# Kernel optimization log

Measured on AMD Instinct MI355X. Metric: run time of the kernel, lower is better.

The kernel has to match this reference:

```python
import jax, jax.numpy as jnp
import numpy as np

HIDDEN = 1024
HEADS = 16
HEAD_DIM = HIDDEN // HEADS


def setup_inputs() -> dict:
    key = jax.random.key(0)
    ks = jax.random.split(key, 9)
    s = 1.0 / np.sqrt(HIDDEN)
    return {
        "x": jax.random.normal(ks[0], (2, 2048, HIDDEN), dtype=jnp.float32),
        "Wq": jax.random.uniform(ks[1], (HIDDEN, HIDDEN), jnp.float32, -s, s),
        "bq": jax.random.uniform(ks[2], (HIDDEN,), jnp.float32, -s, s),
        "Wk": jax.random.uniform(ks[3], (HIDDEN, HIDDEN), jnp.float32, -s, s),
        "bk": jax.random.uniform(ks[4], (HIDDEN,), jnp.float32, -s, s),
        "Wv": jax.random.uniform(ks[5], (HIDDEN, HIDDEN), jnp.float32, -s, s),
        "bv": jax.random.uniform(ks[6], (HIDDEN,), jnp.float32, -s, s),
        "Wo": jax.random.uniform(ks[7], (HIDDEN, HIDDEN), jnp.float32, -s, s),
        "bo": jax.random.uniform(ks[8], (HIDDEN,), jnp.float32, -s, s),
    }


def reference(x, Wq, bq, Wk, bk, Wv, bv, Wo, bo):
    B, N, C = x.shape
    H, D = HEADS, HEAD_DIM
    # torch Linear: y = x @ W.T + b; weights here stored as (out, in)
    q = (x @ Wq.T + bq).reshape(B, N, H, D).transpose(0, 2, 1, 3)  # bhnd
    k = (x @ Wk.T + bk).reshape(B, N, H, D).transpose(0, 2, 1, 3)
    v = (x @ Wv.T + bv).reshape(B, N, H, D).transpose(0, 2, 1, 3)
    scale = D ** -0.5
    attn = jnp.einsum("bhnd,bhmd->bhnm", q, k) * scale
    attn = jax.nn.softmax(attn, axis=-1)
    out = jnp.einsum("bhnm,bhmd->bhnd", attn, v)
    out = out.transpose(0, 2, 1, 3).reshape(B, N, C)
    return out @ Wo.T + bo
```

## Files before the change

kernel.cpp:

```cpp
#include <hip/hip_runtime.h>
#include <stdint.h>

#define HIDDEN 1024
#define HEADS 16
#define HEAD_DIM 64
#define NBATCH 2
#define SEQ 2048

typedef short bh8 __attribute__((ext_vector_type(8)));
typedef _Float16 hf4 __attribute__((ext_vector_type(4)));
typedef _Float16 hf8 __attribute__((ext_vector_type(8)));
typedef float fx4 __attribute__((ext_vector_type(4)));

#define MFMA_BF16(a, b, c) __builtin_amdgcn_mfma_f32_16x16x32_bf16((a), (b), (c), 0, 0, 0)
#define MFMA_F16_16(a, b, c) __builtin_amdgcn_mfma_f32_16x16x16f16((a), (b), (c), 0, 0, 0)

__device__ __forceinline__ short f2bf(float f) {
  union { float f; uint32_t u; } v; v.f = f;
  uint32_t r = v.u + 0x7fffu + ((v.u >> 16) & 1u);
  return (short)(r >> 16);
}
__device__ __forceinline__ short f2h(float f) {
  union { _Float16 h; short s; } v; v.h = (_Float16)f;
  return v.s;
}

typedef __attribute__((address_space(1))) void GV;
typedef __attribute__((address_space(3))) void LV;
__device__ __forceinline__ void gl_lds16(const void* g, void* l) {
  __builtin_amdgcn_global_load_lds((GV*)g, (LV*)l, 16, 0, 0);
}

__device__ __forceinline__ size_t img_off(int row, int k) {
  int rt = row >> 7, kt = k >> 6;
  int g = (((row & 127) >> 4) << 1) + ((k & 63) >> 5);
  int l = (((k & 31) >> 3) << 4) + (row & 15);
  return ((size_t)((rt * 16 + kt) * 16 + g) << 9) + (l << 3) + (k & 7);
}

__global__ void cvt_kernel(const float* __restrict__ x,
                           const float* __restrict__ wq, const float* __restrict__ wk,
                           const float* __restrict__ wv, const float* __restrict__ wo,
                           short* __restrict__ xb, short* __restrict__ wqb,
                           short* __restrict__ wkb, short* __restrict__ wvb,
                           short* __restrict__ wob) {
  long t = (long)blockIdx.x * blockDim.x + threadIdx.x;
  long i = t * 8;
  const float* s; short* d; long off;
  if (i < 4194304L) { s = x; d = xb; off = i; }
  else {
    long j = i - 4194304L;
    int w = (int)(j >> 20);
    off = j & 1048575L;
    s = (w == 0) ? wq : (w == 1) ? wk : (w == 2) ? wv : wo;
    d = (w == 0) ? wqb : (w == 1) ? wkb : (w == 2) ? wvb : wob;
  }
  float4 v0 = *(const float4*)(s + off);
  float4 v1 = *(const float4*)(s + off + 4);
  bh8 o;
  o[0] = f2bf(v0.x); o[1] = f2bf(v0.y); o[2] = f2bf(v0.z); o[3] = f2bf(v0.w);
  o[4] = f2bf(v1.x); o[5] = f2bf(v1.y); o[6] = f2bf(v1.z); o[7] = f2bf(v1.w);
  int row = (int)(off >> 10), k = (int)(off & 1023);
  *(bh8*)(d + img_off(row, k)) = o;
}

__global__ __launch_bounds__(256)
void qkv_kernel(const short* __restrict__ xb,
                const short* __restrict__ wqb, const short* __restrict__ wkb,
                const short* __restrict__ wvb,
                const float* __restrict__ bq, const float* __restrict__ bk,
                const float* __restrict__ bv,
                short* __restrict__ Q, short* __restrict__ K, short* __restrict__ Vt) {
  __shared__ __align__(16) short smem[16384];
  short* Alds = smem;
  short* Blds = smem + 8192;

  const int lin = blockIdx.x;
  const int xcd = lin & 7, idx = lin >> 3;
  const int mt = (xcd >> 1) * 8 + (idx & 7);
  const int zo = (xcd & 1) * 12 + (idx >> 3);
  const int z = zo >> 3, ot = zo & 7;

  const short* W = (z == 0) ? wqb : (z == 1) ? wkb : wvb;
  const float* bias = (z == 0) ? bq : (z == 1) ? bk : bv;
  const int tid = threadIdx.x;
  const int lane = tid & 63, w = tid >> 6;
  const int r = lane & 15, q = lane >> 4;
  const int wr = w >> 1, wc = w & 1;

  fx4 acc[4][4] = {};

  for (int kt = 0; kt < 16; ++kt) {
#pragma unroll
    for (int i = 0; i < 4; ++i) {
      int c = w * 4 + i;
      gl_lds16(xb + (((size_t)(mt * 16 + kt) * 16 + c) << 9) + lane * 8,
               (char*)Alds + c * 1024);
      gl_lds16(W + (((size_t)(ot * 16 + kt) * 16 + c) << 9) + lane * 8,
               (char*)Blds + c * 1024);
    }
    __syncthreads();
#pragma unroll
    for (int ks = 0; ks < 2; ++ks) {
      bh8 af[4], bf_[4];
#pragma unroll
      for (int ti = 0; ti < 4; ++ti)
        af[ti] = *(const bh8*)&Alds[(((wr * 4 + ti) * 2 + ks) << 9) + lane * 8];
#pragma unroll
      for (int tj = 0; tj < 4; ++tj)
        bf_[tj] = *(const bh8*)&Blds[(((wc * 4 + tj) * 2 + ks) << 9) + lane * 8];
#pragma unroll
      for (int ti = 0; ti < 4; ++ti)
#pragma unroll
        for (int tj = 0; tj < 4; ++tj)
          acc[ti][tj] = MFMA_BF16(af[ti], bf_[tj], acc[ti][tj]);
    }
    __syncthreads();
  }

  const float QS = 0.18033688011112042f;
#pragma unroll
  for (int ti = 0; ti < 4; ++ti)
#pragma unroll
    for (int tj = 0; tj < 4; ++tj)
#pragma unroll
      for (int i = 0; i < 4; ++i) {
        int nl = wr * 64 + ti * 16 + q * 4 + i;
        int cl = wc * 64 + tj * 16 + r;
        int hl = cl >> 6, d = cl & 63;
        float v = acc[ti][tj][i] + bias[ot * 128 + cl];
        short sv; int lo;
        if (z == 0) {
          sv = f2bf(v * QS);
          lo = hl * 8192 + nl * 64 + d;
        } else if (z == 1) {
          sv = f2bf(v);
          int g = ((nl >> 4) << 1) + (d >> 5);
          int lp = (((d & 31) >> 3) << 4) + (nl & 15);
          lo = hl * 8192 + g * 512 + lp * 8 + (d & 7);
        } else {
          sv = f2h(v);
          int dt = d >> 4, rp = d & 15;
          int ks2 = nl >> 4, pi = ks2 >> 1, hh = ks2 & 1;
          int qp = (nl & 15) >> 2, ii = nl & 3;
          lo = hl * 8192 + (dt * 4 + pi) * 512 + (qp * 16 + rp) * 8 + hh * 4 + ii;
        }
        smem[lo] = sv;
      }
  __syncthreads();
  {
    int b = mt >> 4;
    int n0 = (mt & 15) * 128;
    int jj = mt & 15;
    short* dst = (z == 0) ? Q : (z == 1) ? K : Vt;
#pragma unroll
    for (int kk = 0; kk < 8; ++kk) {
      int s = kk * 256 + tid;
      int hl = s >> 10, inner = s & 1023;
      int bh = b * 16 + ot * 2 + hl;
      size_t go = (size_t)bh * 131072 +
                  (z == 0 ? (size_t)n0 * 64 : (size_t)jj * 8192) + (size_t)inner * 8;
      *(int4*)(dst + go) = *(const int4*)(smem + (size_t)s * 8);
    }
  }
}

__global__ __launch_bounds__(512, 4)
void attn_kernel(const short* __restrict__ Q, const short* __restrict__ Kf,
                 const short* __restrict__ Vf, short* __restrict__ A) {
  __shared__ __align__(16) short Klds[2][8192];
  __shared__ __align__(16) short Vlds[2][8192];

  const int lin = blockIdx.x;
  const int xcd = lin & 7, idx = lin >> 3;
  const int bh = xcd + 8 * (idx & 3);
  const int n0 = (idx >> 2) * 128;

  const int tid = threadIdx.x;
  const int lane = tid & 63, w = tid >> 6;
  const int r = lane & 15, q = lane >> 4;

  const short* Qg = Q + (size_t)bh * 131072;
  const short* Kg = Kf + (size_t)bh * 131072;
  const short* Vg = Vf + (size_t)bh * 131072;

  bh8 qf[2];
#pragma unroll
  for (int ks = 0; ks < 2; ++ks)
    qf[ks] = *(const bh8*)(Qg + (size_t)(n0 + w * 16 + r) * 64 + ks * 32 + q * 8);

  fx4 o[4] = {};
  float l_run = 0.f;

#define ATTN_STAGE(j, b)                                                        \
  {                                                                             \
    const short* ktp = Kg + (j) * 8192;                                         \
    const short* vtp = Vg + (j) * 8192;                                         \
    _Pragma("unroll") for (int i = 0; i < 4; ++i) {                             \
      if (w < 4) {                                                              \
        int c = w * 4 + i;                                                      \
        gl_lds16(ktp + c * 512 + lane * 8, (char*)&Klds[b][0] + c * 1024);      \
      } else {                                                                  \
        int c = (w - 4) * 4 + i;                                                \
        gl_lds16(vtp + c * 512 + lane * 8, (char*)&Vlds[b][0] + c * 1024);      \
      }                                                                         \
    }                                                                           \
  }

  ATTN_STAGE(0, 0);
  __syncthreads();

  for (int j = 0; j < 16; ++j) {
    int cur = j & 1;
    if (j < 15) ATTN_STAGE(j + 1, cur ^ 1);

    fx4 s[8] = {};
#pragma unroll
    for (int ks = 0; ks < 2; ++ks)
#pragma unroll
      for (int tj = 0; tj < 8; ++tj) {
        bh8 kf = *(const bh8*)&Klds[cur][(tj * 2 + ks) * 512 + lane * 8];
        s[tj] = MFMA_BF16(kf, qf[ks], s[tj]);
      }

    hf4 p[8];
#pragma unroll
    for (int tj = 0; tj < 8; ++tj)
#pragma unroll
      for (int i = 0; i < 4; ++i) {
        float e = __builtin_amdgcn_exp2f(s[tj][i]);
        l_run += e;
        p[tj][i] = (_Float16)e;
      }

#pragma unroll
    for (int pi = 0; pi < 4; ++pi)
#pragma unroll
      for (int dt = 0; dt < 4; ++dt) {
        hf8 vv = *(const hf8*)&Vlds[cur][(dt * 4 + pi) * 512 + lane * 8];
        hf4 vlo = __builtin_shufflevector(vv, vv, 0, 1, 2, 3);
        hf4 vhi = __builtin_shufflevector(vv, vv, 4, 5, 6, 7);
        o[dt] = MFMA_F16_16(vlo, p[2 * pi], o[dt]);
        o[dt] = MFMA_F16_16(vhi, p[2 * pi + 1], o[dt]);
      }
    __syncthreads();
  }
#undef ATTN_STAGE

  float l = l_run;
  l += __shfl_xor(l, 16);
  l += __shfl_xor(l, 32);
  const float inv = 1.0f / l;

  const int h = bh & 15;
  const int mt = (bh >> 4) * 16 + (n0 >> 7);
#pragma unroll
  for (int dt = 0; dt < 4; ++dt) {
    short4 ov;
    ov.x = f2bf(o[dt][0] * inv);
    ov.y = f2bf(o[dt][1] * inv);
    ov.z = f2bf(o[dt][2] * inv);
    ov.w = f2bf(o[dt][3] * inv);
    int g = w * 2 + (dt >> 1);
    int lp = ((dt & 1) * 2 + (q >> 1)) * 16 + r;
    *(short4*)(A + (((size_t)(mt * 16 + h) * 16 + g) << 9) + lp * 8 + (q & 1) * 4) = ov;
  }
}

__global__ __launch_bounds__(256)
void proj_kernel(const short* __restrict__ ab, const short* __restrict__ wob,
                 const float* __restrict__ bo, float* __restrict__ out) {
  __shared__ __align__(16) short Alds[4096];
  __shared__ __align__(16) short Blds[4096];

  const int lin = blockIdx.x;
  const int xcd = lin & 7, idx = lin >> 3;
  const int mt = xcd * 8 + (idx & 7);
  const int ot = idx >> 3;

  const int tid = threadIdx.x;
  const int lane = tid & 63, w = tid >> 6;
  const int r = lane & 15, q = lane >> 4;
  const int wm = w & 1, wn = w >> 1;
  const int rt = mt >> 1, rh = mt & 1;
  const int st = ot >> 1, sh = ot & 1;

  fx4 acc[2][2] = {};

  for (int kt = 0; kt < 16; ++kt) {
#pragma unroll
    for (int i = 0; i < 2; ++i) {
      int c = w * 2 + i;
      gl_lds16(ab + (((size_t)(rt * 16 + kt) * 16 + rh * 8 + c) << 9) + lane * 8,
               (char*)Alds + c * 1024);
      gl_lds16(wob + (((size_t)(st * 16 + kt) * 16 + sh * 8 + c) << 9) + lane * 8,
               (char*)Blds + c * 1024);
    }
    __syncthreads();
#pragma unroll
    for (int ks = 0; ks < 2; ++ks) {
      bh8 af[2], bf_[2];
#pragma unroll
      for (int tm = 0; tm < 2; ++tm)
        af[tm] = *(const bh8*)&Alds[(((wm * 2 + tm) * 2 + ks) << 9) + lane * 8];
#pragma unroll
      for (int tn = 0; tn < 2; ++tn)
        bf_[tn] = *(const bh8*)&Blds[(((wn * 2 + tn) * 2 + ks) << 9) + lane * 8];
#pragma unroll
      for (int tm = 0; tm < 2; ++tm)
#pragma unroll
        for (int tn = 0; tn < 2; ++tn)
          acc[tm][tn] = MFMA_BF16(af[tm], bf_[tn], acc[tm][tn]);
    }
    __syncthreads();
  }

#pragma unroll
  for (int tm = 0; tm < 2; ++tm)
#pragma unroll
    for (int tn = 0; tn < 2; ++tn)
#pragma unroll
      for (int i = 0; i < 4; ++i) {
        int row = mt * 64 + wm * 32 + tm * 16 + q * 4 + i;
        int col = ot * 64 + wn * 32 + tn * 16 + r;
        out[(size_t)row * 1024 + col] = acc[tm][tn][i] + bo[col];
      }
}

extern "C" void kernel_launch(void* const* d_in, const int* in_sizes, int n_in,
                              void* d_out, int out_size, void* d_ws, size_t ws_size,
                              hipStream_t stream) {
  const float* x  = (const float*)d_in[0];
  const float* Wq = (const float*)d_in[1];
  const float* bq = (const float*)d_in[2];
  const float* Wk = (const float*)d_in[3];
  const float* bk = (const float*)d_in[4];
  const float* Wv = (const float*)d_in[5];
  const float* bv = (const float*)d_in[6];
  const float* Wo = (const float*)d_in[7];
  const float* bo = (const float*)d_in[8];
  float* out = (float*)d_out;
  char* ws = (char*)d_ws;

  short* xb  = (short*)(ws);
  short* wqb = (short*)(ws + 8388608);
  short* wkb = (short*)(ws + 8388608 + 2097152);
  short* wvb = (short*)(ws + 8388608 + 2 * 2097152);
  short* wob = (short*)(ws + 8388608 + 3 * 2097152);
  short* Qb  = (short*)(ws + 16777216);
  short* Kb  = (short*)(ws + 16777216 + 8388608);
  short* Vtb = (short*)(ws + 16777216 + 2 * 8388608);
  short* Ab  = (short*)(ws);

  cvt_kernel<<<4096, 256, 0, stream>>>(x, Wq, Wk, Wv, Wo, xb, wqb, wkb, wvb, wob);
  qkv_kernel<<<768, 256, 0, stream>>>(xb, wqb, wkb, wvb, bq, bk, bv, Qb, Kb, Vtb);
  attn_kernel<<<512, 512, 0, stream>>>(Qb, Kb, Vtb, Ab);
  proj_kernel<<<1024, 256, 0, stream>>>(Ab, wob, bo, out);
}
```

Baseline: 198.4 us.

## Double-buffer LDS tiles in QKV and projection GEMMs, widen QKV blocks to 8 waves

```diff
diff --git a/kernel.cpp b/kernel.cpp
--- a/kernel.cpp
+++ b/kernel.cpp
@@ -64,16 +64,14 @@
   *(bh8*)(d + img_off(row, k)) = o;
 }
 
-__global__ __launch_bounds__(256)
+__global__ __launch_bounds__(512)
 void qkv_kernel(const short* __restrict__ xb,
                 const short* __restrict__ wqb, const short* __restrict__ wkb,
                 const short* __restrict__ wvb,
                 const float* __restrict__ bq, const float* __restrict__ bk,
                 const float* __restrict__ bv,
                 short* __restrict__ Q, short* __restrict__ K, short* __restrict__ Vt) {
-  __shared__ __align__(16) short smem[16384];
-  short* Alds = smem;
-  short* Blds = smem + 8192;
+  __shared__ __align__(16) short smem[32768];
 
   const int lin = blockIdx.x;
   const int xcd = lin & 7, idx = lin >> 3;
@@ -86,49 +84,61 @@
   const int tid = threadIdx.x;
   const int lane = tid & 63, w = tid >> 6;
   const int r = lane & 15, q = lane >> 4;
-  const int wr = w >> 1, wc = w & 1;
-
-  fx4 acc[4][4] = {};
+  const int wr = w & 3, wc = w >> 2;
+
+  fx4 acc[2][4] = {};
+
+#define QKV_STAGE(kt, b)                                                            \
+  {                                                                                 \
+    _Pragma("unroll") for (int i = 0; i < 4; ++i) {                                 \
+      int c = w * 4 + i;                                                            \
+      if (c < 16)                                                                   \
+        gl_lds16(xb + (((size_t)(mt * 16 + (kt)) * 16 + c) << 9) + lane * 8,        \
+                 (char*)smem + (size_t)(b) * 16384 + c * 1024);                     \
+      else                                                                          \
+        gl_lds16(W + (((size_t)(ot * 16 + (kt)) * 16 + (c - 16)) << 9) + lane * 8,  \
+                 (char*)smem + 32768 + (size_t)(b) * 16384 + (c - 16) * 1024);      \
+    }                                                                               \
+  }
+
+  QKV_STAGE(0, 0);
+  __syncthreads();
 
   for (int kt = 0; kt < 16; ++kt) {
-#pragma unroll
-    for (int i = 0; i < 4; ++i) {
-      int c = w * 4 + i;
-      gl_lds16(xb + (((size_t)(mt * 16 + kt) * 16 + c) << 9) + lane * 8,
-               (char*)Alds + c * 1024);
-      gl_lds16(W + (((size_t)(ot * 16 + kt) * 16 + c) << 9) + lane * 8,
-               (char*)Blds + c * 1024);
+    int cur = kt & 1;
+    if (kt < 15) QKV_STAGE(kt + 1, cur ^ 1);
+    const short* Ab_ = smem + cur * 8192;
+    const short* Bb_ = smem + 16384 + cur * 8192;
+#pragma unroll
+    for (int ks = 0; ks < 2; ++ks) {
+      bh8 af[2], bf_[4];
+#pragma unroll
+      for (int tm = 0; tm < 2; ++tm)
+        af[tm] = *(const bh8*)&Ab_[(((wr * 2 + tm) * 2 + ks) << 9) + lane * 8];
+#pragma unroll
+      for (int tn = 0; tn < 4; ++tn)
+        bf_[tn] = *(const bh8*)&Bb_[(((wc * 4 + tn) * 2 + ks) << 9) + lane * 8];
+#pragma unroll
+      for (int tm = 0; tm < 2; ++tm)
+#pragma unroll
+        for (int tn = 0; tn < 4; ++tn)
+          acc[tm][tn] = MFMA_BF16(af[tm], bf_[tn], acc[tm][tn]);
     }
     __syncthreads();
-#pragma unroll
-    for (int ks = 0; ks < 2; ++ks) {
-      bh8 af[4], bf_[4];
-#pragma unroll
-      for (int ti = 0; ti < 4; ++ti)
-        af[ti] = *(const bh8*)&Alds[(((wr * 4 + ti) * 2 + ks) << 9) + lane * 8];
-#pragma unroll
-      for (int tj = 0; tj < 4; ++tj)
-        bf_[tj] = *(const bh8*)&Blds[(((wc * 4 + tj) * 2 + ks) << 9) + lane * 8];
-#pragma unroll
-      for (int ti = 0; ti < 4; ++ti)
-#pragma unroll
-        for (int tj = 0; tj < 4; ++tj)
-          acc[ti][tj] = MFMA_BF16(af[ti], bf_[tj], acc[ti][tj]);
-    }
-    __syncthreads();
-  }
+  }
+#undef QKV_STAGE
 
   const float QS = 0.18033688011112042f;
 #pragma unroll
-  for (int ti = 0; ti < 4; ++ti)
-#pragma unroll
-    for (int tj = 0; tj < 4; ++tj)
+  for (int tm = 0; tm < 2; ++tm)
+#pragma unroll
+    for (int tn = 0; tn < 4; ++tn)
 #pragma unroll
       for (int i = 0; i < 4; ++i) {
-        int nl = wr * 64 + ti * 16 + q * 4 + i;
-        int cl = wc * 64 + tj * 16 + r;
+        int nl = wr * 32 + tm * 16 + q * 4 + i;
+        int cl = wc * 64 + tn * 16 + r;
         int hl = cl >> 6, d = cl & 63;
-        float v = acc[ti][tj][i] + bias[ot * 128 + cl];
+        float v = acc[tm][tn][i] + bias[ot * 128 + cl];
         short sv; int lo;
         if (z == 0) {
           sv = f2bf(v * QS);
@@ -154,8 +164,8 @@
     int jj = mt & 15;
     short* dst = (z == 0) ? Q : (z == 1) ? K : Vt;
 #pragma unroll
-    for (int kk = 0; kk < 8; ++kk) {
-      int s = kk * 256 + tid;
+    for (int kk = 0; kk < 4; ++kk) {
+      int s = kk * 512 + tid;
       int hl = s >> 10, inner = s & 1023;
       int bh = b * 16 + ot * 2 + hl;
       size_t go = (size_t)bh * 131072 +
@@ -270,8 +280,8 @@
 __global__ __launch_bounds__(256)
 void proj_kernel(const short* __restrict__ ab, const short* __restrict__ wob,
                  const float* __restrict__ bo, float* __restrict__ out) {
-  __shared__ __align__(16) short Alds[4096];
-  __shared__ __align__(16) short Blds[4096];
+  __shared__ __align__(16) short Alds[2][4096];
+  __shared__ __align__(16) short Blds[2][4096];
 
   const int lin = blockIdx.x;
   const int xcd = lin & 7, idx = lin >> 3;
@@ -287,25 +297,34 @@
 
   fx4 acc[2][2] = {};
 
+#define PROJ_STAGE(kt, b)                                                            \
+  {                                                                                  \
+    _Pragma("unroll") for (int i = 0; i < 4; ++i) {                                  \
+      int c = w * 4 + i;                                                             \
+      if (c < 8)                                                                     \
+        gl_lds16(ab + (((size_t)(rt * 16 + (kt)) * 16 + rh * 8 + c) << 9) + lane * 8,\
+                 (char*)&Alds[b][0] + c * 1024);                                     \
+      else                                                                           \
+        gl_lds16(wob + (((size_t)(st * 16 + (kt)) * 16 + sh * 8 + (c - 8)) << 9) + lane * 8, \
+                 (char*)&Blds[b][0] + (c - 8) * 1024);                               \
+    }                                                                                \
+  }
+
+  PROJ_STAGE(0, 0);
+  __syncthreads();
+
   for (int kt = 0; kt < 16; ++kt) {
-#pragma unroll
-    for (int i = 0; i < 2; ++i) {
-      int c = w * 2 + i;
-      gl_lds16(ab + (((size_t)(rt * 16 + kt) * 16 + rh * 8 + c) << 9) + lane * 8,
-               (char*)Alds + c * 1024);
-      gl_lds16(wob + (((size_t)(st * 16 + kt) * 16 + sh * 8 + c) << 9) + lane * 8,
-               (char*)Blds + c * 1024);
-    }
-    __syncthreads();
+    int cur = kt & 1;
+    if (kt < 15) PROJ_STAGE(kt + 1, cur ^ 1);
 #pragma unroll
     for (int ks = 0; ks < 2; ++ks) {
       bh8 af[2], bf_[2];
 #pragma unroll
       for (int tm = 0; tm < 2; ++tm)
-        af[tm] = *(const bh8*)&Alds[(((wm * 2 + tm) * 2 + ks) << 9) + lane * 8];
+        af[tm] = *(const bh8*)&Alds[cur][(((wm * 2 + tm) * 2 + ks) << 9) + lane * 8];
 #pragma unroll
       for (int tn = 0; tn < 2; ++tn)
-        bf_[tn] = *(const bh8*)&Blds[(((wn * 2 + tn) * 2 + ks) << 9) + lane * 8];
+        bf_[tn] = *(const bh8*)&Blds[cur][(((wn * 2 + tn) * 2 + ks) << 9) + lane * 8];
 #pragma unroll
       for (int tm = 0; tm < 2; ++tm)
 #pragma unroll
@@ -314,6 +333,7 @@
     }
     __syncthreads();
   }
+#undef PROJ_STAGE
 
 #pragma unroll
   for (int tm = 0; tm < 2; ++tm)
@@ -353,7 +373,7 @@
   short* Ab  = (short*)(ws);
 
   cvt_kernel<<<4096, 256, 0, stream>>>(x, Wq, Wk, Wv, Wo, xb, wqb, wkb, wvb, wob);
-  qkv_kernel<<<768, 256, 0, stream>>>(xb, wqb, wkb, wvb, bq, bk, bv, Qb, Kb, Vtb);
+  qkv_kernel<<<768, 512, 0, stream>>>(xb, wqb, wkb, wvb, bq, bk, bv, Qb, Kb, Vtb);
   attn_kernel<<<512, 512, 0, stream>>>(Qb, Kb, Vtb, Ab);
   proj_kernel<<<1024, 256, 0, stream>>>(Ab, wob, bo, out);
 }
```

New measurement: 186.1 us. 6.2% less time.
